# Optimization experiments

Measured on AMD Instinct MI355X. Metric: run time of the kernel, lower is better.

Reference implementation:

```python
import jax, jax.numpy as jnp
import numpy as np

B, N, TASK_DIM, HW_DIM, EMB = 32768, 32, 17, 16, 64


def _w(key, shape, scale=0.1):
    return jax.random.normal(key, shape, dtype=jnp.float32) * scale


def setup_inputs() -> dict:
    key = jax.random.key(0)
    ks = jax.random.split(key, 24)
    inp = {
        "task_vecs": jax.random.normal(ks[0], (B, TASK_DIM), dtype=jnp.float32),
        "hw_vecs": jax.random.normal(ks[1], (B, N, HW_DIM), dtype=jnp.float32),
        "valid_mask": jnp.ones((B, N), dtype=bool),
        # TaskEncoder: Linear(17,64) ReLU Linear(64,64) ReLU
        "te_w1": _w(ks[2], (TASK_DIM, 64)), "te_b1": jnp.zeros((64,), jnp.float32),
        "te_w2": _w(ks[3], (64, EMB)),      "te_b2": jnp.zeros((EMB,), jnp.float32),
        # HWEncoder: Linear(16,64) ReLU Linear(64,64) ReLU
        "he_w1": _w(ks[4], (HW_DIM, 64)),   "he_b1": jnp.zeros((64,), jnp.float32),
        "he_w2": _w(ks[5], (64, EMB)),      "he_b2": jnp.zeros((EMB,), jnp.float32),
        # Scorer: Linear(128,64) ReLU Linear(64,32) ReLU Linear(32,1)
        "sc_w1": _w(ks[6], (2 * EMB, 64)),  "sc_b1": jnp.zeros((64,), jnp.float32),
        "sc_w2": _w(ks[7], (64, 32)),       "sc_b2": jnp.zeros((32,), jnp.float32),
        "sc_w3": _w(ks[8], (32, 1)),        "sc_b3": jnp.zeros((1,), jnp.float32),
        # RejectHead: Linear(64,32) ReLU Linear(32,1)
        "rj_w1": _w(ks[9], (EMB, 32)),      "rj_b1": jnp.zeros((32,), jnp.float32),
        "rj_w2": _w(ks[10], (32, 1)),       "rj_b2": jnp.zeros((1,), jnp.float32),
        # ValueHead: Linear(128,64) ReLU Linear(64,1)
        "vh_w1": _w(ks[11], (2 * EMB, 64)), "vh_b1": jnp.zeros((64,), jnp.float32),
        "vh_w2": _w(ks[12], (64, 1)),       "vh_b2": jnp.zeros((1,), jnp.float32),
    }
    return inp


def reference(task_vecs, hw_vecs, valid_mask,
              te_w1, te_b1, te_w2, te_b2,
              he_w1, he_b1, he_w2, he_b2,
              sc_w1, sc_b1, sc_w2, sc_b2, sc_w3, sc_b3,
              rj_w1, rj_b1, rj_w2, rj_b2,
              vh_w1, vh_b1, vh_w2, vh_b2):
    relu = jax.nn.relu
    # task embedding [B, EMB]
    task_emb = relu(relu(task_vecs @ te_w1 + te_b1) @ te_w2 + te_b2)
    # hw embeddings [B, N, EMB]
    hw_emb = relu(relu(hw_vecs @ he_w1 + he_b1) @ he_w2 + he_b2)
    # scorer on concat(task_emb, hw_emb) -> [B, N]
    comb = jnp.concatenate(
        [jnp.broadcast_to(task_emb[:, None, :], hw_emb.shape), hw_emb], axis=-1)
    h = relu(comb @ sc_w1 + sc_b1)
    h = relu(h @ sc_w2 + sc_b2)
    hw_scores = (h @ sc_w3 + sc_b3)[..., 0]  # [B, N]
    # reject score [B]
    reject = (relu(task_emb @ rj_w1 + rj_b1) @ rj_w2 + rj_b2)[..., 0]
    all_scores = jnp.concatenate([hw_scores, reject[:, None]], axis=1)  # [B, N+1]
    # mask (reject slot always valid)
    full_mask = jnp.concatenate(
        [valid_mask, jnp.ones((valid_mask.shape[0], 1), dtype=bool)], axis=1)
    all_scores = jnp.where(full_mask, all_scores, -jnp.inf)
    action_probs = jax.nn.softmax(all_scores, axis=1)
    # value head on concat(task_emb, mean hw_emb)
    mean_hw = hw_emb.mean(axis=1)
    vin = jnp.concatenate([task_emb, mean_hw], axis=1)
    value = (relu(vin @ vh_w1 + vh_b1) @ vh_w2 + vh_b2)[..., 0]  # [B]
    return action_probs, value, all_scores
```

## Files before the change

kernel.cpp:

```cpp
#include <hip/hip_runtime.h>
#include <hip/hip_bf16.h>

typedef __attribute__((ext_vector_type(8))) short bfrag;
typedef __attribute__((ext_vector_type(4))) float vf4;

#define MFMA16(A,B,C) __builtin_amdgcn_mfma_f32_16x16x32_bf16(A,B,C,0,0,0)

struct KParams {
  const float* task; const float* hw; const int* mask;
  const float* te_w1; const float* te_b1; const float* te_w2; const float* te_b2;
  const float* he_w1; const float* he_b1; const float* he_w2; const float* he_b2;
  const float* sc_w1; const float* sc_b1; const float* sc_w2; const float* sc_b2;
  const float* sc_w3; const float* sc_b3;
  const float* rj_w1; const float* rj_b1; const float* rj_w2; const float* rj_b2;
  const float* vh_w1; const float* vh_b1; const float* vh_w2; const float* vh_b2;
  float* out; float* ws; int B;
};

__device__ __forceinline__ unsigned pack2(float a, float b){
  __hip_bfloat162 h = __float22bfloat162_rn(make_float2(a,b));
  unsigned u; __builtin_memcpy(&u, &h, 4); return u;
}

__device__ __forceinline__ float frag_elem(const KParams& P, int fid, int lane, int e){
  const float* W; const float* bias = nullptr; int OUT = 64, KREAL, c, q = 0;
  if (fid < 4)       { W=P.te_w1; bias=P.te_b1; KREAL=17; c=fid; }
  else if (fid < 12) { W=P.te_w2;              KREAL=64; int t=fid-4;  c=t>>1; q=t&1; }
  else if (fid < 20) { W=P.sc_w1;              KREAL=64; int t=fid-12; c=t>>1; q=t&1; }
  else if (fid < 28) { W=P.vh_w1;              KREAL=64; int t=fid-20; c=t>>1; q=t&1; }
  else if (fid < 32) { W=P.rj_w1; OUT=32;      KREAL=64; int t=fid-28; c=t>>1; q=t&1; }
  else if (fid < 36) { W=P.he_w1; bias=P.he_b1; KREAL=16; c=fid-32; }
  else if (fid < 44) { W=P.he_w2;              KREAL=64; int t=fid-36; c=t>>1; q=t&1; }
  else if (fid < 52) { W=P.sc_w1 + 64*64;      KREAL=64; int t=fid-44; c=t>>1; q=t&1; }
  else if (fid < 56) { W=P.sc_w2; OUT=32;      KREAL=64; int t=fid-52; c=t>>1; q=t&1; }
  else               { W=P.vh_w1 + 64*64;      KREAL=64; int t=fid-56; c=t>>1; q=t&1; }
  int row = c*16 + (lane & 15);
  int k   = q*32 + ((e>>2)<<4) + ((lane>>4)<<2) + (e&3);
  if (k < KREAL) return W[k*OUT + row];
  if (k == KREAL && bias) return bias[row];
  return 0.f;
}

__device__ __forceinline__ float chunk_elem(const KParams& P, int cid, int lane, int r){
  const float* src; int base;
  if (cid < 4)       { src=P.te_b2; base=cid*16; }
  else if (cid < 8)  { src=P.sc_b1; base=(cid-4)*16; }
  else if (cid < 12) { src=P.vh_b1; base=(cid-8)*16; }
  else if (cid < 14) { src=P.rj_b1; base=(cid-12)*16; }
  else if (cid < 18) { src=P.he_b2; base=(cid-14)*16; }
  else if (cid < 20) { src=P.sc_b2; base=(cid-18)*16; }
  else if (cid < 22) { src=P.sc_w3; base=(cid-20)*16; }
  else if (cid < 24) { src=P.rj_w2; base=(cid-22)*16; }
  else               { src=P.vh_w2; base=(cid-24)*16; }
  return src[base + ((lane>>4)<<2) + r];
}

__global__ void setup_frags(KParams P){
  int l = threadIdx.x, bid = blockIdx.x;
  if (bid < 64){
    uint4 u;
    u.x = pack2(frag_elem(P,bid,l,0), frag_elem(P,bid,l,1));
    u.y = pack2(frag_elem(P,bid,l,2), frag_elem(P,bid,l,3));
    u.z = pack2(frag_elem(P,bid,l,4), frag_elem(P,bid,l,5));
    u.w = pack2(frag_elem(P,bid,l,6), frag_elem(P,bid,l,7));
    ((uint4*)P.ws)[bid*64 + l] = u;
  } else {
    int cid = bid - 64;
    float4 v;
    v.x = chunk_elem(P,cid,l,0); v.y = chunk_elem(P,cid,l,1);
    v.z = chunk_elem(P,cid,l,2); v.w = chunk_elem(P,cid,l,3);
    ((float4*)(P.ws + 16384))[cid*64 + l] = v;
  }
}

template<int WS>
__device__ __forceinline__ bfrag load_frag(const KParams& P, int fid, int l){
  union { uint4 q; bfrag v; } X;
  if (WS) X.q = ((const uint4*)P.ws)[fid*64 + l];
  else {
    X.q.x = pack2(frag_elem(P,fid,l,0), frag_elem(P,fid,l,1));
    X.q.y = pack2(frag_elem(P,fid,l,2), frag_elem(P,fid,l,3));
    X.q.z = pack2(frag_elem(P,fid,l,4), frag_elem(P,fid,l,5));
    X.q.w = pack2(frag_elem(P,fid,l,6), frag_elem(P,fid,l,7));
  }
  return X.v;
}
template<int WS>
__device__ __forceinline__ vf4 load_chunk(const KParams& P, int cid, int l){
  vf4 r;
  if (WS){
    float4 t = ((const float4*)(P.ws + 16384))[cid*64 + l];
    r[0]=t.x; r[1]=t.y; r[2]=t.z; r[3]=t.w;
  } else {
    r[0]=chunk_elem(P,cid,l,0); r[1]=chunk_elem(P,cid,l,1);
    r[2]=chunk_elem(P,cid,l,2); r[3]=chunk_elem(P,cid,l,3);
  }
  return r;
}

template<bool RELU>
__device__ __forceinline__ bfrag packAB(vf4 A, vf4 B){
  if (RELU){
    #pragma unroll
    for (int i=0;i<4;i++){ A[i]=fmaxf(A[i],0.f); B[i]=fmaxf(B[i],0.f); }
  }
  union { unsigned u[4]; bfrag v; } X;
  X.u[0]=pack2(A[0],A[1]); X.u[1]=pack2(A[2],A[3]);
  X.u[2]=pack2(B[0],B[1]); X.u[3]=pack2(B[2],B[3]);
  return X.v;
}

template<int WS>
__global__ __launch_bounds__(256,2) void fused_policy(KParams P){
  __shared__ float lds_v [4][16][64];
  __shared__ float lds_sc[4][16][33];
  __shared__ float lds_pr[4][16][33];
  __shared__ float lds_inv[4][16];
  const int tid = threadIdx.x;
  const int wid = tid>>6, l = tid&63, col = l&15, grp = l>>4;
  const int b0  = (blockIdx.x*4 + wid)*16;
  const vf4 Z = {0.f,0.f,0.f,0.f};

  const float* tp = P.task + (size_t)(b0+col)*17;
  union { unsigned u[4]; bfrag v; } TB;
  TB.u[0]=pack2(tp[grp*4+0],tp[grp*4+1]);
  TB.u[1]=pack2(tp[grp*4+2],tp[grp*4+3]);
  TB.u[2]= (grp==0) ? pack2(tp[16], 1.f) : 0u;
  TB.u[3]=0u;
  vf4 a1[4];
  #pragma unroll
  for (int c=0;c<4;c++) a1[c] = MFMA16(load_frag<WS>(P,c,l), TB.v, Z);
  bfrag h1B0 = packAB<true>(a1[0],a1[1]), h1B1 = packAB<true>(a1[2],a1[3]);
  vf4 a2[4];
  #pragma unroll
  for (int c=0;c<4;c++){
    a2[c] = MFMA16(load_frag<WS>(P,4+2*c,l), h1B0, load_chunk<WS>(P,c,l));
    a2[c] = MFMA16(load_frag<WS>(P,5+2*c,l), h1B1, a2[c]);
  }
  bfrag teB0 = packAB<true>(a2[0],a2[1]), teB1 = packAB<true>(a2[2],a2[3]);
  vf4 tc[4];
  #pragma unroll
  for (int c=0;c<4;c++){
    tc[c] = MFMA16(load_frag<WS>(P,12+2*c,l), teB0, load_chunk<WS>(P,4+c,l));
    tc[c] = MFMA16(load_frag<WS>(P,13+2*c,l), teB1, tc[c]);
  }
  #pragma unroll
  for (int c=0;c<4;c++){
    vf4 vc = MFMA16(load_frag<WS>(P,20+2*c,l), teB0, load_chunk<WS>(P,8+c,l));
    vc = MFMA16(load_frag<WS>(P,21+2*c,l), teB1, vc);
    *(float4*)&lds_v[wid][col][c*16+grp*4] = make_float4(vc[0],vc[1],vc[2],vc[3]);
  }
  float rpart = 0.f;
  #pragma unroll
  for (int c=0;c<2;c++){
    vf4 rv = MFMA16(load_frag<WS>(P,28+2*c,l), teB0, load_chunk<WS>(P,12+c,l));
    rv = MFMA16(load_frag<WS>(P,29+2*c,l), teB1, rv);
    vf4 w2 = load_chunk<WS>(P,22+c,l);
    #pragma unroll
    for (int r=0;r<4;r++) rpart += fmaxf(rv[r],0.f)*w2[r];
  }
  rpart += __shfl_xor(rpart,16);
  rpart += __shfl_xor(rpart,32);
  const float reject = rpart + P.rj_b2[0];

  bfrag Fhe1[4], Fhe2[8], Fs1[8], Fs2[4];
  #pragma unroll
  for (int i=0;i<4;i++) Fhe1[i]=load_frag<WS>(P,32+i,l);
  #pragma unroll
  for (int i=0;i<8;i++) Fhe2[i]=load_frag<WS>(P,36+i,l);
  #pragma unroll
  for (int i=0;i<8;i++) Fs1[i]=load_frag<WS>(P,44+i,l);
  #pragma unroll
  for (int i=0;i<4;i++) Fs2[i]=load_frag<WS>(P,52+i,l);
  vf4 Bhe2[4], Bsc2[2], W3[2];
  #pragma unroll
  for (int c=0;c<4;c++) Bhe2[c]=load_chunk<WS>(P,14+c,l);
  #pragma unroll
  for (int c=0;c<2;c++) Bsc2[c]=load_chunk<WS>(P,18+c,l);
  #pragma unroll
  for (int c=0;c<2;c++) W3[c]=load_chunk<WS>(P,20+c,l);
  const float scb3 = P.sc_b3[0];
  vf4 macc[4];
  #pragma unroll
  for (int c=0;c<4;c++) macc[c]=Z;

  const float* hwp = P.hw + (size_t)(b0+col)*512 + grp*4;
  float4 hv = *(const float4*)hwp;
  #pragma unroll 1
  for (int n=0;n<32;n++){
    float4 hv_next = hv;
    if (n < 31) hv_next = *(const float4*)(hwp + (n+1)*16);
    union { unsigned u[4]; bfrag v; } HB;
    HB.u[0]=pack2(hv.x,hv.y); HB.u[1]=pack2(hv.z,hv.w);
    HB.u[2]= (grp==0) ? pack2(1.f,0.f) : 0u;
    HB.u[3]=0u;
    vf4 g1[4];
    #pragma unroll
    for (int c=0;c<4;c++) g1[c]=MFMA16(Fhe1[c], HB.v, Z);
    bfrag g1B0 = packAB<true>(g1[0],g1[1]), g1B1 = packAB<true>(g1[2],g1[3]);
    vf4 g2[4];
    #pragma unroll
    for (int c=0;c<4;c++){
      g2[c]=MFMA16(Fhe2[2*c],   g1B0, Bhe2[c]);
      g2[c]=MFMA16(Fhe2[2*c+1], g1B1, g2[c]);
      #pragma unroll
      for (int r=0;r<4;r++){ g2[c][r]=fmaxf(g2[c][r],0.f); macc[c][r]+=g2[c][r]; }
    }
    bfrag g2B0 = packAB<false>(g2[0],g2[1]), g2B1 = packAB<false>(g2[2],g2[3]);
    vf4 s1[4];
    #pragma unroll
    for (int c=0;c<4;c++){
      s1[c]=MFMA16(Fs1[2*c],   g2B0, tc[c]);
      s1[c]=MFMA16(Fs1[2*c+1], g2B1, s1[c]);
    }
    bfrag s1B0 = packAB<true>(s1[0],s1[1]), s1B1 = packAB<true>(s1[2],s1[3]);
    float sp = 0.f;
    #pragma unroll
    for (int c=0;c<2;c++){
      vf4 s2 = MFMA16(Fs2[2*c],   s1B0, Bsc2[c]);
      s2     = MFMA16(Fs2[2*c+1], s1B1, s2);
      #pragma unroll
      for (int r=0;r<4;r++) sp += fmaxf(s2[r],0.f)*W3[c][r];
    }
    sp += __shfl_xor(sp,16);
    sp += __shfl_xor(sp,32);
    if (l<16) lds_sc[wid][l][n] = sp + scb3;
    hv = hv_next;
  }
  if (l<16) lds_sc[wid][l][32] = reject;

  #pragma unroll
  for (int c=0;c<4;c++){
    #pragma unroll
    for (int r=0;r<4;r++) macc[c][r] *= (1.f/32.f);
  }
  bfrag mB0 = packAB<false>(macc[0],macc[1]), mB1 = packAB<false>(macc[2],macc[3]);
  asm volatile("s_waitcnt lgkmcnt(0)" ::: "memory");
  float vpart = 0.f;
  #pragma unroll
  for (int c=0;c<4;c++){
    float4 ci4 = *(const float4*)&lds_v[wid][col][c*16+grp*4];
    vf4 ci = {ci4.x,ci4.y,ci4.z,ci4.w};
    vf4 vD = MFMA16(load_frag<WS>(P,56+2*c,l), mB0, ci);
    vD     = MFMA16(load_frag<WS>(P,57+2*c,l), mB1, vD);
    vf4 w2 = load_chunk<WS>(P,24+c,l);
    #pragma unroll
    for (int r=0;r<4;r++) vpart += fmaxf(vD[r],0.f)*w2[r];
  }
  vpart += __shfl_xor(vpart,16);
  vpart += __shfl_xor(vpart,32);
  if (l<16) P.out[(size_t)P.B*33 + b0 + l] = vpart + P.vh_b2[0];

  asm volatile("s_waitcnt lgkmcnt(0)" ::: "memory");
  if (l<16){
    float s[33];
    #pragma unroll
    for (int j=0;j<32;j++) s[j]=lds_sc[wid][l][j];
    s[32]=reject;
    const int4* mp = (const int4*)(P.mask + (size_t)(b0+l)*32);
    #pragma unroll
    for (int w=0;w<8;w++){
      int4 m4 = mp[w];
      if (m4.x==0) s[w*4+0] = -INFINITY;
      if (m4.y==0) s[w*4+1] = -INFINITY;
      if (m4.z==0) s[w*4+2] = -INFINITY;
      if (m4.w==0) s[w*4+3] = -INFINITY;
    }
    #pragma unroll
    for (int j=0;j<32;j++) lds_sc[wid][l][j] = s[j];
    float mx = s[32];
    #pragma unroll
    for (int j=0;j<32;j++) mx = fmaxf(mx, s[j]);
    float sum = 0.f;
    #pragma unroll
    for (int j=0;j<33;j++){
      float p = __expf(s[j]-mx); sum += p; lds_pr[wid][l][j] = p;
    }
    lds_inv[wid][l] = 1.f/sum;
  }
  asm volatile("s_waitcnt lgkmcnt(0)" ::: "memory");
  const float* prf = &lds_pr[wid][0][0];
  const float* scf = &lds_sc[wid][0][0];
  #pragma unroll 1
  for (int i=l; i<528; i+=64){
    unsigned bl = (unsigned)i/33u;
    P.out[(size_t)b0*33 + i]                      = prf[i]*lds_inv[wid][bl];
    P.out[(size_t)P.B*34 + (size_t)b0*33 + i]     = scf[i];
  }
}

extern "C" void kernel_launch(void* const* d_in, const int* in_sizes, int n_in,
                              void* d_out, int out_size, void* d_ws, size_t ws_size,
                              hipStream_t stream){
  KParams P;
  P.task  = (const float*)d_in[0];
  P.hw    = (const float*)d_in[1];
  P.mask  = (const int*)d_in[2];
  P.te_w1 = (const float*)d_in[3];  P.te_b1 = (const float*)d_in[4];
  P.te_w2 = (const float*)d_in[5];  P.te_b2 = (const float*)d_in[6];
  P.he_w1 = (const float*)d_in[7];  P.he_b1 = (const float*)d_in[8];
  P.he_w2 = (const float*)d_in[9];  P.he_b2 = (const float*)d_in[10];
  P.sc_w1 = (const float*)d_in[11]; P.sc_b1 = (const float*)d_in[12];
  P.sc_w2 = (const float*)d_in[13]; P.sc_b2 = (const float*)d_in[14];
  P.sc_w3 = (const float*)d_in[15]; P.sc_b3 = (const float*)d_in[16];
  P.rj_w1 = (const float*)d_in[17]; P.rj_b1 = (const float*)d_in[18];
  P.rj_w2 = (const float*)d_in[19]; P.rj_b2 = (const float*)d_in[20];
  P.vh_w1 = (const float*)d_in[21]; P.vh_b1 = (const float*)d_in[22];
  P.vh_w2 = (const float*)d_in[23]; P.vh_b2 = (const float*)d_in[24];
  P.out = (float*)d_out;
  P.ws  = (float*)d_ws;
  P.B   = in_sizes[0] / 17;
  const size_t need = 64u*1024u + 28u*1024u;
  const bool use_ws = (d_ws != nullptr) && (ws_size >= need);
  if (use_ws){
    setup_frags<<<92, 64, 0, stream>>>(P);
    fused_policy<1><<<P.B/64, 256, 0, stream>>>(P);
  } else {
    fused_policy<0><<<P.B/64, 256, 0, stream>>>(P);
  }
}
```

Baseline: 57.91 us.

## Stage loop weights in LDS and process two HW slots per iteration

The 24 per-slot weight fragments are moved out of registers into shared memory, loaded once per block and read back with ds_read inside the loop. The N loop is unrolled by two so the two independent MFMA chains interleave and hide dependency latency. The value-head intermediate now stays in registers instead of a shared-memory round trip. Register pressure should fall and ILP rise, at the cost of extra LDS traffic per iteration and a block-wide barrier.

```diff
diff --git a/kernel.cpp b/kernel.cpp
--- a/kernel.cpp
+++ b/kernel.cpp
@@ -110,9 +110,13 @@
   return X.v;
 }
 
+__device__ __forceinline__ bfrag ldsF(const uint4* lw, int j, int l){
+  union { uint4 q; bfrag v; } X; X.q = lw[j*64 + l]; return X.v;
+}
+
 template<int WS>
 __global__ __launch_bounds__(256,2) void fused_policy(KParams P){
-  __shared__ float lds_v [4][16][64];
+  __shared__ uint4 lds_w[24*64];
   __shared__ float lds_sc[4][16][33];
   __shared__ float lds_pr[4][16][33];
   __shared__ float lds_inv[4][16];
@@ -121,6 +125,22 @@
   const int b0  = (blockIdx.x*4 + wid)*16;
   const vf4 Z = {0.f,0.f,0.f,0.f};
 
+  if (WS){
+    const uint4* w4 = (const uint4*)P.ws;
+    #pragma unroll
+    for (int i=0;i<6;i++) lds_w[tid + i*256] = w4[32*64 + tid + i*256];
+  } else {
+    for (int i=tid; i<24*64; i+=256){
+      int fid = 32 + (i>>6), lane = i&63;
+      uint4 u;
+      u.x = pack2(frag_elem(P,fid,lane,0), frag_elem(P,fid,lane,1));
+      u.y = pack2(frag_elem(P,fid,lane,2), frag_elem(P,fid,lane,3));
+      u.z = pack2(frag_elem(P,fid,lane,4), frag_elem(P,fid,lane,5));
+      u.w = pack2(frag_elem(P,fid,lane,6), frag_elem(P,fid,lane,7));
+      lds_w[i] = u;
+    }
+  }
+
   const float* tp = P.task + (size_t)(b0+col)*17;
   union { unsigned u[4]; bfrag v; } TB;
   TB.u[0]=pack2(tp[grp*4+0],tp[grp*4+1]);
@@ -144,11 +164,11 @@
     tc[c] = MFMA16(load_frag<WS>(P,12+2*c,l), teB0, load_chunk<WS>(P,4+c,l));
     tc[c] = MFMA16(load_frag<WS>(P,13+2*c,l), teB1, tc[c]);
   }
-  #pragma unroll
-  for (int c=0;c<4;c++){
-    vf4 vc = MFMA16(load_frag<WS>(P,20+2*c,l), teB0, load_chunk<WS>(P,8+c,l));
-    vc = MFMA16(load_frag<WS>(P,21+2*c,l), teB1, vc);
-    *(float4*)&lds_v[wid][col][c*16+grp*4] = make_float4(vc[0],vc[1],vc[2],vc[3]);
+  vf4 vc[4];
+  #pragma unroll
+  for (int c=0;c<4;c++){
+    vc[c] = MFMA16(load_frag<WS>(P,20+2*c,l), teB0, load_chunk<WS>(P,8+c,l));
+    vc[c] = MFMA16(load_frag<WS>(P,21+2*c,l), teB1, vc[c]);
   }
   float rpart = 0.f;
   #pragma unroll
@@ -163,15 +183,6 @@
   rpart += __shfl_xor(rpart,32);
   const float reject = rpart + P.rj_b2[0];
 
-  bfrag Fhe1[4], Fhe2[8], Fs1[8], Fs2[4];
-  #pragma unroll
-  for (int i=0;i<4;i++) Fhe1[i]=load_frag<WS>(P,32+i,l);
-  #pragma unroll
-  for (int i=0;i<8;i++) Fhe2[i]=load_frag<WS>(P,36+i,l);
-  #pragma unroll
-  for (int i=0;i<8;i++) Fs1[i]=load_frag<WS>(P,44+i,l);
-  #pragma unroll
-  for (int i=0;i<4;i++) Fs2[i]=load_frag<WS>(P,52+i,l);
   vf4 Bhe2[4], Bsc2[2], W3[2];
   #pragma unroll
   for (int c=0;c<4;c++) Bhe2[c]=load_chunk<WS>(P,14+c,l);
@@ -184,48 +195,79 @@
   #pragma unroll
   for (int c=0;c<4;c++) macc[c]=Z;
 
+  __syncthreads();
+
   const float* hwp = P.hw + (size_t)(b0+col)*512 + grp*4;
-  float4 hv = *(const float4*)hwp;
+  float4 hvA = *(const float4*)(hwp);
+  float4 hvB = *(const float4*)(hwp + 16);
   #pragma unroll 1
-  for (int n=0;n<32;n++){
-    float4 hv_next = hv;
-    if (n < 31) hv_next = *(const float4*)(hwp + (n+1)*16);
-    union { unsigned u[4]; bfrag v; } HB;
-    HB.u[0]=pack2(hv.x,hv.y); HB.u[1]=pack2(hv.z,hv.w);
-    HB.u[2]= (grp==0) ? pack2(1.f,0.f) : 0u;
-    HB.u[3]=0u;
-    vf4 g1[4];
-    #pragma unroll
-    for (int c=0;c<4;c++) g1[c]=MFMA16(Fhe1[c], HB.v, Z);
-    bfrag g1B0 = packAB<true>(g1[0],g1[1]), g1B1 = packAB<true>(g1[2],g1[3]);
-    vf4 g2[4];
+  for (int n=0;n<32;n+=2){
+    float4 nA = hvA, nB = hvB;
+    if (n < 30){
+      nA = *(const float4*)(hwp + (n+2)*16);
+      nB = *(const float4*)(hwp + (n+3)*16);
+    }
+    union { unsigned u[4]; bfrag v; } H0, H1;
+    H0.u[0]=pack2(hvA.x,hvA.y); H0.u[1]=pack2(hvA.z,hvA.w);
+    H0.u[2]= (grp==0) ? pack2(1.f,0.f) : 0u;
+    H0.u[3]=0u;
+    H1.u[0]=pack2(hvB.x,hvB.y); H1.u[1]=pack2(hvB.z,hvB.w);
+    H1.u[2]=H0.u[2]; H1.u[3]=0u;
+
+    vf4 g1a[4], g1b[4];
     #pragma unroll
     for (int c=0;c<4;c++){
-      g2[c]=MFMA16(Fhe2[2*c],   g1B0, Bhe2[c]);
-      g2[c]=MFMA16(Fhe2[2*c+1], g1B1, g2[c]);
+      bfrag f = ldsF(lds_w, c, l);
+      g1a[c]=MFMA16(f, H0.v, Z);
+      g1b[c]=MFMA16(f, H1.v, Z);
+    }
+    bfrag g1aB0 = packAB<true>(g1a[0],g1a[1]), g1aB1 = packAB<true>(g1a[2],g1a[3]);
+    bfrag g1bB0 = packAB<true>(g1b[0],g1b[1]), g1bB1 = packAB<true>(g1b[2],g1b[3]);
+
+    vf4 g2a[4], g2b[4];
+    #pragma unroll
+    for (int c=0;c<4;c++){
+      bfrag f0 = ldsF(lds_w, 4+2*c, l), f1 = ldsF(lds_w, 5+2*c, l);
+      g2a[c]=MFMA16(f1, g1aB1, MFMA16(f0, g1aB0, Bhe2[c]));
+      g2b[c]=MFMA16(f1, g1bB1, MFMA16(f0, g1bB0, Bhe2[c]));
       #pragma unroll
-      for (int r=0;r<4;r++){ g2[c][r]=fmaxf(g2[c][r],0.f); macc[c][r]+=g2[c][r]; }
-    }
-    bfrag g2B0 = packAB<false>(g2[0],g2[1]), g2B1 = packAB<false>(g2[2],g2[3]);
-    vf4 s1[4];
+      for (int r=0;r<4;r++){
+        g2a[c][r]=fmaxf(g2a[c][r],0.f); g2b[c][r]=fmaxf(g2b[c][r],0.f);
+        macc[c][r] += g2a[c][r] + g2b[c][r];
+      }
+    }
+    bfrag g2aB0 = packAB<false>(g2a[0],g2a[1]), g2aB1 = packAB<false>(g2a[2],g2a[3]);
+    bfrag g2bB0 = packAB<false>(g2b[0],g2b[1]), g2bB1 = packAB<false>(g2b[2],g2b[3]);
+
+    vf4 s1a[4], s1b[4];
     #pragma unroll
     for (int c=0;c<4;c++){
-      s1[c]=MFMA16(Fs1[2*c],   g2B0, tc[c]);
-      s1[c]=MFMA16(Fs1[2*c+1], g2B1, s1[c]);
-    }
-    bfrag s1B0 = packAB<true>(s1[0],s1[1]), s1B1 = packAB<true>(s1[2],s1[3]);
-    float sp = 0.f;
+      bfrag f0 = ldsF(lds_w, 12+2*c, l), f1 = ldsF(lds_w, 13+2*c, l);
+      s1a[c]=MFMA16(f1, g2aB1, MFMA16(f0, g2aB0, tc[c]));
+      s1b[c]=MFMA16(f1, g2bB1, MFMA16(f0, g2bB0, tc[c]));
+    }
+    bfrag s1aB0 = packAB<true>(s1a[0],s1a[1]), s1aB1 = packAB<true>(s1a[2],s1a[3]);
+    bfrag s1bB0 = packAB<true>(s1b[0],s1b[1]), s1bB1 = packAB<true>(s1b[2],s1b[3]);
+
+    float sp0 = 0.f, sp1 = 0.f;
     #pragma unroll
     for (int c=0;c<2;c++){
-      vf4 s2 = MFMA16(Fs2[2*c],   s1B0, Bsc2[c]);
-      s2     = MFMA16(Fs2[2*c+1], s1B1, s2);
+      bfrag f0 = ldsF(lds_w, 20+2*c, l), f1 = ldsF(lds_w, 21+2*c, l);
+      vf4 s2a = MFMA16(f1, s1aB1, MFMA16(f0, s1aB0, Bsc2[c]));
+      vf4 s2b = MFMA16(f1, s1bB1, MFMA16(f0, s1bB0, Bsc2[c]));
       #pragma unroll
-      for (int r=0;r<4;r++) sp += fmaxf(s2[r],0.f)*W3[c][r];
-    }
-    sp += __shfl_xor(sp,16);
-    sp += __shfl_xor(sp,32);
-    if (l<16) lds_sc[wid][l][n] = sp + scb3;
-    hv = hv_next;
+      for (int r=0;r<4;r++){
+        sp0 += fmaxf(s2a[r],0.f)*W3[c][r];
+        sp1 += fmaxf(s2b[r],0.f)*W3[c][r];
+      }
+    }
+    sp0 += __shfl_xor(sp0,16); sp0 += __shfl_xor(sp0,32);
+    sp1 += __shfl_xor(sp1,16); sp1 += __shfl_xor(sp1,32);
+    if (l<16){
+      lds_sc[wid][l][n]   = sp0 + scb3;
+      lds_sc[wid][l][n+1] = sp1 + scb3;
+    }
+    hvA = nA; hvB = nB;
   }
   if (l<16) lds_sc[wid][l][32] = reject;
 
@@ -235,13 +277,10 @@
     for (int r=0;r<4;r++) macc[c][r] *= (1.f/32.f);
   }
   bfrag mB0 = packAB<false>(macc[0],macc[1]), mB1 = packAB<false>(macc[2],macc[3]);
-  asm volatile("s_waitcnt lgkmcnt(0)" ::: "memory");
   float vpart = 0.f;
   #pragma unroll
   for (int c=0;c<4;c++){
-    float4 ci4 = *(const float4*)&lds_v[wid][col][c*16+grp*4];
-    vf4 ci = {ci4.x,ci4.y,ci4.z,ci4.w};
-    vf4 vD = MFMA16(load_frag<WS>(P,56+2*c,l), mB0, ci);
+    vf4 vD = MFMA16(load_frag<WS>(P,56+2*c,l), mB0, vc[c]);
     vD     = MFMA16(load_frag<WS>(P,57+2*c,l), mB1, vD);
     vf4 w2 = load_chunk<WS>(P,24+c,l);
     #pragma unroll
```

Result: slower. 59.82 us (+3.3%).
